# Kernel tuning notes

Measured on AMD Instinct MI355X. Metric: run time of the kernel, lower is better.

Reference implementation:

```python
import jax, jax.numpy as jnp
import numpy as np

N_HEADS = 16


def setup_inputs() -> dict:
    key = jax.random.key(0)
    k1, k2, k3 = jax.random.split(key, 3)
    d = 1024
    x = jax.random.normal(k1, (8, 1024, d), dtype=jnp.float32)
    w_qkv = jax.random.normal(k2, (d, 3 * d), dtype=jnp.float32) * (1.0 / np.sqrt(d))
    w_out = jax.random.normal(k3, (d, d), dtype=jnp.float32) * (1.0 / np.sqrt(d))
    b_out = jnp.zeros((d,), dtype=jnp.float32)
    return {"x": x, "w_qkv": w_qkv, "w_out": w_out, "b_out": b_out}


def reference(x, w_qkv, w_out, b_out):
    a, b, c = x.shape
    h = N_HEADS
    hd = c // h
    scale = 1.0 / (c ** 0.5)  # note: 1/sqrt(model_dim), not head_dim
    qkv = (x @ w_qkv).reshape(a, b, 3, h, hd)
    q, k, v = jnp.moveaxis(qkv, 2, 0)          # each (a, b, h, hd)
    q = jnp.swapaxes(q, 1, 2)                  # (a, h, b, hd)
    k = jnp.swapaxes(k, 1, 2)
    v = jnp.swapaxes(v, 1, 2)
    scores = jnp.einsum('ahqd,ahkd->ahqk', q, k) * scale  # (a, h, b, b)
    # Faithful to the source: softmax over dim=1 (the HEADS axis)
    attn = jax.nn.softmax(scores, axis=1)
    out = jnp.einsum('ahqk,ahkd->ahqd', attn, v)           # (a, h, b, hd)
    out = jnp.swapaxes(out, 1, 2).reshape(a, b, c)
    return out @ w_out + b_out
```

## Files before the change

### kernel.cpp

```cpp
#include <hip/hip_runtime.h>
#include <hip/hip_bf16.h>

typedef __attribute__((ext_vector_type(8))) short short8;
typedef __attribute__((ext_vector_type(4))) short short4e;
typedef __attribute__((ext_vector_type(4))) float f32x4;
typedef __attribute__((ext_vector_type(16))) float f32x16;
typedef __attribute__((ext_vector_type(4))) unsigned uint4v;

#define SC_LOG2E 0.04508422f
#define MFMA32(a, b, c) __builtin_amdgcn_mfma_f32_32x32x16_bf16(a, b, c, 0, 0, 0)

__device__ inline short bf16r(float f) {
    union { float f; unsigned u; } v; v.f = f;
    unsigned r = v.u + 0x7FFFu + ((v.u >> 16) & 1u);
    return (short)(r >> 16);
}
__device__ inline float bflo(unsigned u) {
    union { unsigned u; float f; } v; v.u = u << 16; return v.f;
}
__device__ inline float bfhi(unsigned u) {
    union { unsigned u; float f; } v; v.u = u & 0xffff0000u; return v.f;
}
#if __has_builtin(__builtin_amdgcn_exp2f)
__device__ inline float fexp2(float x) { return __builtin_amdgcn_exp2f(x); }
#else
__device__ inline float fexp2(float x) { return __expf(x * 0.6931471806f); }
#endif
__device__ inline unsigned cvt_pk_bf16(float lo, float hi) {
    unsigned r;
    asm("v_cvt_pk_bf16_f32 %0, %1, %2" : "=v"(r) : "v"(lo), "v"(hi));
    return r;
}
__device__ inline void perm32swap(unsigned& a, unsigned& b) {
    asm("v_permlane32_swap_b32 %0, %1" : "+v"(a), "+v"(b));
}

#define GLOAD_LDS16(gp, lp) __builtin_amdgcn_global_load_lds( \
    (const __attribute__((address_space(1))) unsigned int*)(gp), \
    (__attribute__((address_space(3))) unsigned int*)(lp), 16, 0, 0)

#define WB10 do { asm volatile("s_waitcnt vmcnt(10)\ns_barrier" ::: "memory"); __builtin_amdgcn_sched_barrier(0); } while (0)
#define WB4  do { asm volatile("s_waitcnt vmcnt(4)\ns_barrier"  ::: "memory"); __builtin_amdgcn_sched_barrier(0); } while (0)
#define WB0  do { asm volatile("s_waitcnt vmcnt(0)\ns_barrier"  ::: "memory"); __builtin_amdgcn_sched_barrier(0); } while (0)

__global__ void castk(const float* __restrict__ in, short* __restrict__ out, int n4) {
    int i = blockIdx.x * 256 + threadIdx.x;
    if (i < n4) {
        float4 v = ((const float4*)in)[i];
        short4 o;
        o.x = bf16r(v.x); o.y = bf16r(v.y); o.z = bf16r(v.z); o.w = bf16r(v.w);
        ((short4*)out)[i] = o;
    }
}

__global__ void tcast(const float* __restrict__ src, short* __restrict__ dst, int R, int C,
                      int nscale, float sfac) {
    __shared__ float tile[32][33];
    int bi = blockIdx.x, bj = blockIdx.y;
    int tx = threadIdx.x & 31, ty = threadIdx.x >> 5;
#pragma unroll
    for (int p = 0; p < 4; p++)
        tile[ty + p * 8][tx] = src[(long)(bi * 32 + ty + p * 8) * C + bj * 32 + tx];
    __syncthreads();
#pragma unroll
    for (int p = 0; p < 4; p++) {
        int n = bj * 32 + ty + p * 8;
        float v = tile[tx][ty + p * 8];
        if (n < nscale) v *= sfac;
        dst[(long)n * R + bi * 32 + tx] = bf16r(v);
    }
}

__global__ __launch_bounds__(512, 2)
void gemm256(const short* __restrict__ A, const short* __restrict__ Bt,
             short* __restrict__ qkv, short* __restrict__ Vt) {
    __shared__ short lds[65536];
    const int wg = blockIdx.x;
    const int lg = (wg & 7) * 48 + (wg >> 3);
    const int bx = lg % 12, by = lg / 12;
    const int m0 = by * 256, n0 = bx * 256;
    const int tid = threadIdx.x, w = tid >> 6, lane = tid & 63;
    const int wm = w >> 2, wn = w & 3;
    const int l15 = lane & 15, lhi = lane >> 4;
    f32x4 acc[8][4] = {};

    auto stA = [&](int t, int ks) {
#pragma unroll
        for (int j = 0; j < 2; j++) {
            int c = j * 512 + tid;
            int row = c >> 2, sl = c & 3;
            GLOAD_LDS16(A + (long)(m0 + row) * 1024 + t * 64 + ks * 32 + ((sl ^ ((row >> 1) & 3)) * 8),
                        &lds[((t & 1) * 2 + ks) * 8192 + c * 8]);
        }
    };
    auto stB = [&](int t, int ks) {
#pragma unroll
        for (int j = 0; j < 2; j++) {
            int c = j * 512 + tid;
            int row = c >> 2, sl = c & 3;
            GLOAD_LDS16(Bt + (long)(n0 + row) * 1024 + t * 64 + ks * 32 + ((sl ^ ((row >> 1) & 3)) * 8),
                        &lds[32768 + ((t & 1) * 2 + ks) * 8192 + c * 8]);
        }
    };

    short8 af[8], bf[2];
    auto ldA = [&](int buf, int ks) {
#pragma unroll
        for (int fi = 0; fi < 8; fi++) {
            int row = wm * 128 + fi * 16 + l15;
            af[fi] = *(const short8*)(&lds[(buf * 2 + ks) * 8192 + row * 32 +
                                           ((lhi ^ ((row >> 1) & 3)) * 8)]);
        }
    };
    auto ldB = [&](int buf, int ks, int fh) {
#pragma unroll
        for (int u = 0; u < 2; u++) {
            int row = wn * 64 + (fh * 2 + u) * 16 + l15;
            bf[u] = *(const short8*)(&lds[32768 + (buf * 2 + ks) * 8192 + row * 32 +
                                          ((lhi ^ ((row >> 1) & 3)) * 8)]);
        }
    };
    auto mm = [&](int fh) {
        __builtin_amdgcn_s_setprio(1);
#pragma unroll
        for (int fi = 0; fi < 8; fi++)
#pragma unroll
            for (int u = 0; u < 2; u++)
                acc[fi][fh * 2 + u] = __builtin_amdgcn_mfma_f32_16x16x32_bf16(
                    af[fi], bf[u], acc[fi][fh * 2 + u], 0, 0, 0);
        __builtin_amdgcn_s_setprio(0);
    };

    stA(0, 0); stB(0, 0); stA(0, 1); stB(0, 1); stA(1, 0); stB(1, 0);

    for (int i = 0; i < 8; i++) {
        const int t0 = 2 * i;
        stA(t0 + 1, 1); WB10;
        ldA(0, 0); ldB(0, 0, 0); mm(0);
        stB(t0 + 1, 1); WB10;
        ldB(0, 0, 1); mm(1);
        if (i < 7) stA(t0 + 2, 0);
        WB10;
        ldA(0, 1); ldB(0, 1, 0); mm(0);
        if (i < 7) stB(t0 + 2, 0);
        WB10;
        ldB(0, 1, 1); mm(1);
        if (i < 7) { stA(t0 + 2, 1); WB10; } else { WB4; }
        ldA(1, 0); ldB(1, 0, 0); mm(0);
        if (i < 7) { stB(t0 + 2, 1); WB10; } else { WB4; }
        ldB(1, 0, 1); mm(1);
        if (i < 7) { stA(t0 + 3, 0); WB10; } else { WB0; }
        ldA(1, 1); ldB(1, 1, 0); mm(0);
        if (i < 7) { stB(t0 + 3, 0); WB10; } else { WB0; }
        ldB(1, 1, 1); mm(1);
    }

    if (n0 >= 2048) {
        const int a = m0 >> 10, k0v = m0 & 1023;
#pragma unroll
        for (int fi = 0; fi < 8; fi++)
#pragma unroll
            for (int fj = 0; fj < 4; fj++) {
                int colp = n0 - 2048 + wn * 64 + fj * 16 + l15;
                int k = k0v + wm * 128 + fi * 16 + lhi * 4;
                short4e s4;
#pragma unroll
                for (int r = 0; r < 4; r++) s4[r] = bf16r(acc[fi][fj][r]);
                *(short4e*)(Vt + (long)a * 1048576 + (long)colp * 1024 + k) = s4;
            }
    } else {
#pragma unroll
        for (int fi = 0; fi < 8; fi++)
#pragma unroll
            for (int fj = 0; fj < 4; fj++)
#pragma unroll
                for (int r = 0; r < 4; r++) {
                    int row = m0 + wm * 128 + fi * 16 + lhi * 4 + r;
                    int col = n0 + wn * 64 + fj * 16 + l15;
                    qkv[(long)row * 3072 + col] = bf16r(acc[fi][fj][r]);
                }
    }
}

template<int OUT_BF16>
__global__ __launch_bounds__(256, 3)
void gemm_bt(const short* __restrict__ A, const short* __restrict__ Bt,
             void* __restrict__ Cout, const float* __restrict__ bias,
             int M, int N, int K, int nbx, int cpx, int lda) {
    __shared__ short As[3][128 * 32];
    __shared__ short Bs[3][128 * 32];
    const int wg = blockIdx.x;
    const int lg = (wg & 7) * cpx + (wg >> 3);
    const int bx = lg % nbx, by = lg / nbx;
    const int tid = threadIdx.x, w = tid >> 6, lane = tid & 63;
    const int wr = w >> 1, wc = w & 1;
    const int l15 = lane & 15, lhi = lane >> 4;
    const int m0 = by * 128, n0 = bx * 128;
    f32x4 acc[4][4] = {};
    const int NT = K / 32;

    auto stage = [&](int buf, int t) {
        int k0 = t * 32;
#pragma unroll
        for (int j = 0; j < 2; j++) {
            int chunk = w * 128 + j * 64 + lane;
            int row = chunk >> 2, cp = chunk & 3;
            int cc = cp ^ ((row >> 1) & 3);
            GLOAD_LDS16(A  + (long)(m0 + row) * lda + k0 + cc * 8, &As[buf][chunk * 8]);
            GLOAD_LDS16(Bt + (long)(n0 + row) * K   + k0 + cc * 8, &Bs[buf][chunk * 8]);
        }
    };

    stage(0, 0);
    stage(1, 1);
    asm volatile("s_waitcnt vmcnt(4)\ns_barrier" ::: "memory");
    __builtin_amdgcn_sched_barrier(0);

    int bR = 0, bW = 2;
    for (int t = 0; t < NT; t++) {
        bool issued = (t + 2 < NT);
        if (issued) stage(bW, t + 2);
        const short* Ab = As[bR];
        const short* Bb = Bs[bR];
        short8 af[4], bfr[4];
#pragma unroll
        for (int i = 0; i < 4; i++) {
            int arow = wr * 64 + i * 16 + l15;
            int brow = wc * 64 + i * 16 + l15;
            af[i]  = *(const short8*)(Ab + arow * 32 + (lhi ^ ((arow >> 1) & 3)) * 8);
            bfr[i] = *(const short8*)(Bb + brow * 32 + (lhi ^ ((brow >> 1) & 3)) * 8);
        }
        __builtin_amdgcn_s_setprio(1);
#pragma unroll
        for (int i = 0; i < 4; i++)
#pragma unroll
            for (int j = 0; j < 4; j++)
                acc[i][j] = __builtin_amdgcn_mfma_f32_16x16x32_bf16(af[i], bfr[j], acc[i][j], 0, 0, 0);
        __builtin_amdgcn_s_setprio(0);
        if (issued) asm volatile("s_waitcnt vmcnt(4)\ns_barrier" ::: "memory");
        else        asm volatile("s_waitcnt vmcnt(0)\ns_barrier" ::: "memory");
        __builtin_amdgcn_sched_barrier(0);
        bR = (bR == 2) ? 0 : bR + 1;
        bW = (bW == 2) ? 0 : bW + 1;
    }
#pragma unroll
    for (int i = 0; i < 4; i++)
#pragma unroll
        for (int j = 0; j < 4; j++)
#pragma unroll
            for (int r = 0; r < 4; r++) {
                int row = m0 + wr * 64 + i * 16 + lhi * 4 + r;
                int col = n0 + wc * 64 + j * 16 + l15;
                float v = acc[i][j][r];
                if (OUT_BF16) ((short*)Cout)[(long)row * N + col] = bf16r(v);
                else          ((float*)Cout)[(long)row * N + col] = v + bias[col];
            }
}

__global__ __launch_bounds__(256, 2)
void dsum_kernel(const short* __restrict__ qkv, unsigned* __restrict__ negL) {
    __shared__ short Qs[2][128 * 64];
    __shared__ short Ks[2][128 * 64];
    const int wg = blockIdx.x;
    const int lg = (wg & 7) * 64 + (wg >> 3);
    const int a = lg >> 6, q0 = ((lg >> 3) & 7) * 128, k0 = (lg & 7) * 128;
    const int tid = threadIdx.x, w = tid >> 6, lane = tid & 63;
    const int wr = w >> 1, wc = w & 1;
    const int l31 = lane & 31, hi = lane >> 5;
    const long qb = (long)a * 3145728;
    f32x16 dacc[2][2] = {};

    auto stage = [&](int buf, int hh) {
#pragma unroll
        for (int j = 0; j < 4; j++) {
            int c = j * 256 + tid;
            int row = c >> 3, cc = (c & 7) ^ (row & 7);
            GLOAD_LDS16(qkv + qb + (long)(q0 + row) * 3072 + hh * 64 + cc * 8,        &Qs[buf][c * 8]);
            GLOAD_LDS16(qkv + qb + (long)(k0 + row) * 3072 + 1024 + hh * 64 + cc * 8, &Ks[buf][c * 8]);
        }
    };

    stage(0, 0);
    __syncthreads();
    int buf = 0;
    for (int hh = 0; hh < 16; hh++) {
        if (hh < 15) stage(buf ^ 1, hh + 1);
        short8 ka[2][4], qf[2][4];
#pragma unroll
        for (int i = 0; i < 2; i++)
#pragma unroll
            for (int dc = 0; dc < 4; dc++) {
                int row = wr * 64 + i * 32 + l31;
                int ph = (dc * 2 + hi) ^ (row & 7);
                ka[i][dc] = *(const short8*)(&Ks[buf][row * 64 + ph * 8]);
            }
#pragma unroll
        for (int j = 0; j < 2; j++)
#pragma unroll
            for (int dc = 0; dc < 4; dc++) {
                int row = wc * 64 + j * 32 + l31;
                int ph = (dc * 2 + hi) ^ (row & 7);
                qf[j][dc] = *(const short8*)(&Qs[buf][row * 64 + ph * 8]);
            }
#pragma unroll
        for (int i = 0; i < 2; i++)
#pragma unroll
            for (int j = 0; j < 2; j++) {
                f32x16 s = {};
#pragma unroll
                for (int dc = 0; dc < 4; dc++)
                    s = MFMA32(ka[i][dc], qf[j][dc], s);
#pragma unroll
                for (int r = 0; r < 16; r++)
                    dacc[i][j][r] += fexp2(s[r]);
            }
        __syncthreads();
        buf ^= 1;
    }
#pragma unroll
    for (int i = 0; i < 2; i++)
#pragma unroll
        for (int j = 0; j < 2; j++) {
            int ktg = (k0 >> 5) + wr * 2 + i;
            int qtg = (q0 >> 5) + wc * 2 + j;
            unsigned pwv[8];
#pragma unroll
            for (int u = 0; u < 8; u++)
                pwv[u] = cvt_pk_bf16(-__log2f(dacc[i][j][2 * u]),
                                     -__log2f(dacc[i][j][2 * u + 1]));
            unsigned* dst = negL + (((long)(a * 32 + ktg) * 32 + qtg) << 9) + lane * 8;
            *(uint4v*)dst       = (uint4v){pwv[0], pwv[1], pwv[2], pwv[3]};
            *(uint4v*)(dst + 4) = (uint4v){pwv[4], pwv[5], pwv[6], pwv[7]};
        }
}

__global__ __launch_bounds__(256, 2)
void attn2_kernel(const short* __restrict__ qkv, const short* __restrict__ Vt,
                  const unsigned* __restrict__ negL, short* __restrict__ ctx) {
    __shared__ short lds[3 * 8192];
    const int wg = blockIdx.x;
    const int lg = (wg & 7) * 64 + (wg >> 3);
    const int a = lg >> 6, h = (lg >> 2) & 15, qblk = lg & 3;
    const int tid = threadIdx.x, w = tid >> 6, lane = tid & 63;
    const int l31 = lane & 31, hi = lane >> 5;
    const int qw = qblk * 256 + w * 64;
    const long qb = (long)a * 3145728;

    short8 qfrag[2][4];
#pragma unroll
    for (int qs = 0; qs < 2; qs++)
#pragma unroll
        for (int dc = 0; dc < 4; dc++)
            qfrag[qs][dc] = *(const short8*)(qkv + qb +
                (long)(qw + qs * 32 + l31) * 3072 + h * 64 + dc * 16 + hi * 8);

    const short* kcol  = qkv + qb + 1024 + h * 64;
    const short* vbase = Vt + (long)a * 1048576 + (long)(h * 64) * 1024;
    const unsigned* lbase = negL + (long)a * 524288 + (qw >> 5) * 512 + lane * 8;

    auto stage = [&](int buf, int t) {
        int k0 = t * 64;
#pragma unroll
        for (int j = 0; j < 2; j++) {
            GLOAD_LDS16(kcol + (long)(k0 + j * 32 + l31) * 3072 + w * 16 + hi * 8,
                        &lds[buf * 8192 + (j * 256 + tid) * 8]);
            int fidx = j * 4 + w, n = fidx >> 1, dt = fidx & 1;
            GLOAD_LDS16(vbase + (long)(dt * 32 + l31) * 1024 + k0 + n * 16 + hi * 8,
                        &lds[buf * 8192 + 4096 + (j * 256 + tid) * 8]);
        }
    };

    f32x16 oacc[2][2] = {};
    stage(0, 0);
    stage(1, 1);
    asm volatile("s_waitcnt vmcnt(4)\ns_barrier" ::: "memory");
    __builtin_amdgcn_sched_barrier(0);

    int bR = 0, bW = 2;
    for (int t = 0; t < 16; t++) {
        uint4v dm[2][2][2];
#pragma unroll
        for (int qs = 0; qs < 2; qs++)
#pragma unroll
            for (int kt = 0; kt < 2; kt++) {
                const unsigned* dp = lbase + (long)(t * 2 + kt) * 16384 + qs * 512;
                dm[qs][kt][0] = *(const uint4v*)dp;
                dm[qs][kt][1] = *(const uint4v*)(dp + 4);
            }
        if (t + 2 < 16) stage(bW, t + 2);

        const short* Kb = &lds[bR * 8192];
        const short* Vb = &lds[bR * 8192 + 4096];
#pragma unroll
        for (int kt = 0; kt < 2; kt++) {
            short8 ka[4];
#pragma unroll
            for (int dc = 0; dc < 4; dc++)
                ka[dc] = *(const short8*)(Kb + ((kt * 4 + dc) * 64 + lane) * 8);

            short8 pf[2][2];
#pragma unroll
            for (int qs = 0; qs < 2; qs++) {
                f32x16 s = {};
                __builtin_amdgcn_s_setprio(1);
#pragma unroll
                for (int dc = 0; dc < 4; dc++)
                    s = MFMA32(ka[dc], qfrag[qs][dc], s);
                __builtin_amdgcn_s_setprio(0);
                unsigned pw[8];
#pragma unroll
                for (int u = 0; u < 8; u++) {
                    unsigned d = dm[qs][kt][u >> 2][u & 3];
                    float e0 = fexp2(s[2 * u]     + bflo(d));
                    float e1 = fexp2(s[2 * u + 1] + bfhi(d));
                    pw[u] = cvt_pk_bf16(e0, e1);
                }
                perm32swap(pw[0], pw[2]); perm32swap(pw[1], pw[3]);
                perm32swap(pw[4], pw[6]); perm32swap(pw[5], pw[7]);
                union { uint4v u; short8 s8; } c0, c1;
                c0.u = (uint4v){pw[0], pw[1], pw[2], pw[3]};
                c1.u = (uint4v){pw[4], pw[5], pw[6], pw[7]};
                pf[qs][0] = c0.s8;
                pf[qs][1] = c1.s8;
            }
            __builtin_amdgcn_s_setprio(1);
#pragma unroll
            for (int dt = 0; dt < 2; dt++)
#pragma unroll
                for (int nn = 0; nn < 2; nn++) {
                    short8 vf = *(const short8*)(Vb + (((kt * 2 + nn) * 2 + dt) * 64 + lane) * 8);
#pragma unroll
                    for (int qs = 0; qs < 2; qs++)
                        oacc[qs][dt] = MFMA32(pf[qs][nn], vf, oacc[qs][dt]);
                }
            __builtin_amdgcn_s_setprio(0);
        }
        asm volatile("s_waitcnt vmcnt(4)\ns_barrier" ::: "memory");
        __builtin_amdgcn_sched_barrier(0);
        bR = (bR == 2) ? 0 : bR + 1;
        bW = (bW == 2) ? 0 : bW + 1;
    }
#pragma unroll
    for (int qs = 0; qs < 2; qs++)
#pragma unroll
        for (int dt = 0; dt < 2; dt++)
#pragma unroll
            for (int r = 0; r < 16; r++) {
                int q = qw + qs * 32 + (r & 3) + 8 * (r >> 2) + 4 * hi;
                int col = h * 64 + dt * 32 + l31;
                ctx[((long)a * 1024 + q) * 3072 + col] = bf16r(oacc[qs][dt][r]);
            }
}

extern "C" void kernel_launch(void* const* d_in, const int* in_sizes, int n_in,
                              void* d_out, int out_size, void* d_ws, size_t ws_size,
                              hipStream_t stream) {
    const float* x     = (const float*)d_in[0];
    const float* w_qkv = (const float*)d_in[1];
    const float* w_out = (const float*)d_in[2];
    const float* b_out = (const float*)d_in[3];
    float* out = (float*)d_out;

    char* ws = (char*)d_ws;
    short* wqkvT   = (short*)(ws);
    unsigned* negL = (unsigned*)(ws);
    short* xb    = (short*)(ws + 16777216);
    short* woT   = (short*)(ws + 33554432);
    short* qkv   = (short*)(ws + 35651584);
    short* Vt    = (short*)(ws + 85983232);
    short* ctx   = qkv + 2048;
    if (ws_size < 109051904u) return;

    castk<<<8192, 256, 0, stream>>>(x, xb, 2097152);
    tcast<<<dim3(32, 96), 256, 0, stream>>>(w_qkv, wqkvT, 1024, 3072, 1024, SC_LOG2E);
    tcast<<<dim3(32, 32), 256, 0, stream>>>(w_out, woT, 1024, 1024, 0, 1.0f);
    gemm256<<<384, 512, 0, stream>>>(xb, wqkvT, qkv, Vt);
    dsum_kernel<<<512, 256, 0, stream>>>(qkv, negL);
    attn2_kernel<<<512, 256, 0, stream>>>(qkv, Vt, negL, ctx);
    gemm_bt<0><<<512, 256, 0, stream>>>(ctx, woT, (void*)out, b_out, 8192, 1024, 1024, 8, 64, 3072);
}
```

Baseline: 192.5 us.

## Widen QKV GEMM tile to 256x384 so 256 workgroups fill the GPU in one wave

The QKV projection GEMM now uses 256x384 output tiles, which gives 256 workgroups that map one per CU on the 256-CU part instead of 384 tiles running in 1.5 waves. LDS grows to hold the larger B tile, occupancy drops to one workgroup per CU, and the software pipeline is rewritten with a per-k-tile schedule, new vmcnt waits and plain barriers. The epilogue now picks the Vt or qkv store per 16-column fragment, because a tile can straddle the V boundary. The risks are the lost latency hiding from the second resident workgroup and possible errors in the hand-tuned wait counts.

```diff
diff --git a/kernel.cpp b/kernel.cpp
--- a/kernel.cpp
+++ b/kernel.cpp
@@ -39,9 +39,12 @@
     (const __attribute__((address_space(1))) unsigned int*)(gp), \
     (__attribute__((address_space(3))) unsigned int*)(lp), 16, 0, 0)
 
+#define WB12 do { asm volatile("s_waitcnt vmcnt(12)\ns_barrier" ::: "memory"); __builtin_amdgcn_sched_barrier(0); } while (0)
 #define WB10 do { asm volatile("s_waitcnt vmcnt(10)\ns_barrier" ::: "memory"); __builtin_amdgcn_sched_barrier(0); } while (0)
+#define WB5  do { asm volatile("s_waitcnt vmcnt(5)\ns_barrier"  ::: "memory"); __builtin_amdgcn_sched_barrier(0); } while (0)
 #define WB4  do { asm volatile("s_waitcnt vmcnt(4)\ns_barrier"  ::: "memory"); __builtin_amdgcn_sched_barrier(0); } while (0)
 #define WB0  do { asm volatile("s_waitcnt vmcnt(0)\ns_barrier"  ::: "memory"); __builtin_amdgcn_sched_barrier(0); } while (0)
+#define BARO do { asm volatile("s_barrier" ::: "memory"); __builtin_amdgcn_sched_barrier(0); } while (0)
 
 __global__ void castk(const float* __restrict__ in, short* __restrict__ out, int n4) {
     int i = blockIdx.x * 256 + threadIdx.x;
@@ -71,18 +74,19 @@
     }
 }
 
-__global__ __launch_bounds__(512, 2)
+__global__ __launch_bounds__(512, 1)
 void gemm256(const short* __restrict__ A, const short* __restrict__ Bt,
              short* __restrict__ qkv, short* __restrict__ Vt) {
-    __shared__ short lds[65536];
+    __shared__ short lds[81920];
     const int wg = blockIdx.x;
-    const int lg = (wg & 7) * 48 + (wg >> 3);
-    const int bx = lg % 12, by = lg / 12;
-    const int m0 = by * 256, n0 = bx * 256;
+    const int cx = wg & 7, idx = wg >> 3;
+    const int by = (cx & 3) * 8 + (idx & 7);
+    const int bx = (cx >> 2) * 4 + (idx >> 3);
+    const int m0 = by * 256, n0 = bx * 384;
     const int tid = threadIdx.x, w = tid >> 6, lane = tid & 63;
     const int wm = w >> 2, wn = w & 3;
     const int l15 = lane & 15, lhi = lane >> 4;
-    f32x4 acc[8][4] = {};
+    f32x4 acc[8][6] = {};
 
     auto stA = [&](int t, int ks) {
 #pragma unroll
@@ -95,11 +99,11 @@
     };
     auto stB = [&](int t, int ks) {
 #pragma unroll
-        for (int j = 0; j < 2; j++) {
+        for (int j = 0; j < 3; j++) {
             int c = j * 512 + tid;
             int row = c >> 2, sl = c & 3;
             GLOAD_LDS16(Bt + (long)(n0 + row) * 1024 + t * 64 + ks * 32 + ((sl ^ ((row >> 1) & 3)) * 8),
-                        &lds[32768 + ((t & 1) * 2 + ks) * 8192 + c * 8]);
+                        &lds[32768 + ((t & 1) * 2 + ks) * 12288 + c * 8]);
         }
     };
 
@@ -115,8 +119,8 @@
     auto ldB = [&](int buf, int ks, int fh) {
 #pragma unroll
         for (int u = 0; u < 2; u++) {
-            int row = wn * 64 + (fh * 2 + u) * 16 + l15;
-            bf[u] = *(const short8*)(&lds[32768 + (buf * 2 + ks) * 8192 + row * 32 +
+            int row = wn * 96 + (fh * 2 + u) * 16 + l15;
+            bf[u] = *(const short8*)(&lds[32768 + (buf * 2 + ks) * 12288 + row * 32 +
                                           ((lhi ^ ((row >> 1) & 3)) * 8)]);
         }
     };
@@ -131,55 +135,55 @@
         __builtin_amdgcn_s_setprio(0);
     };
 
-    stA(0, 0); stB(0, 0); stA(0, 1); stB(0, 1); stA(1, 0); stB(1, 0);
-
-    for (int i = 0; i < 8; i++) {
-        const int t0 = 2 * i;
-        stA(t0 + 1, 1); WB10;
-        ldA(0, 0); ldB(0, 0, 0); mm(0);
-        stB(t0 + 1, 1); WB10;
-        ldB(0, 0, 1); mm(1);
-        if (i < 7) stA(t0 + 2, 0);
-        WB10;
-        ldA(0, 1); ldB(0, 1, 0); mm(0);
-        if (i < 7) stB(t0 + 2, 0);
-        WB10;
-        ldB(0, 1, 1); mm(1);
-        if (i < 7) { stA(t0 + 2, 1); WB10; } else { WB4; }
-        ldA(1, 0); ldB(1, 0, 0); mm(0);
-        if (i < 7) { stB(t0 + 2, 1); WB10; } else { WB4; }
-        ldB(1, 0, 1); mm(1);
-        if (i < 7) { stA(t0 + 3, 0); WB10; } else { WB0; }
-        ldA(1, 1); ldB(1, 1, 0); mm(0);
-        if (i < 7) { stB(t0 + 3, 0); WB10; } else { WB0; }
-        ldB(1, 1, 1); mm(1);
-    }
-
-    if (n0 >= 2048) {
-        const int a = m0 >> 10, k0v = m0 & 1023;
-#pragma unroll
-        for (int fi = 0; fi < 8; fi++)
-#pragma unroll
-            for (int fj = 0; fj < 4; fj++) {
-                int colp = n0 - 2048 + wn * 64 + fj * 16 + l15;
+    stA(0, 0); stB(0, 0); stA(0, 1); stB(0, 1); stA(1, 0); stB(1, 0); stA(1, 1);
+
+    for (int t = 0; t < 14; t++) {
+        const int b = t & 1;
+        WB12;             ldA(b, 0); ldB(b, 0, 0); mm(0);
+        stB(t + 1, 1); BARO; ldB(b, 0, 1); mm(1);
+        stA(t + 2, 0); BARO; ldB(b, 0, 2); mm(2);
+        WB12;             ldA(b, 1); ldB(b, 1, 0); mm(0);
+        stB(t + 2, 0); BARO; ldB(b, 1, 1); mm(1);
+        stA(t + 2, 1); BARO; ldB(b, 1, 2); mm(2);
+    }
+    {
+        WB12;             ldA(0, 0); ldB(0, 0, 0); mm(0);
+        stB(15, 1); BARO; ldB(0, 0, 1); mm(1);
+        BARO;             ldB(0, 0, 2); mm(2);
+        WB10;             ldA(0, 1); ldB(0, 1, 0); mm(0);
+        BARO;             ldB(0, 1, 1); mm(1);
+        BARO;             ldB(0, 1, 2); mm(2);
+    }
+    {
+        WB5;              ldA(1, 0); ldB(1, 0, 0); mm(0);
+        BARO;             ldB(1, 0, 1); mm(1);
+        BARO;             ldB(1, 0, 2); mm(2);
+        WB0;              ldA(1, 1); ldB(1, 1, 0); mm(0);
+        BARO;             ldB(1, 1, 1); mm(1);
+        BARO;             ldB(1, 1, 2); mm(2);
+    }
+
+    const int a = m0 >> 10, k0v = m0 & 1023;
+#pragma unroll
+    for (int fi = 0; fi < 8; fi++)
+#pragma unroll
+        for (int fj = 0; fj < 6; fj++) {
+            int colb = n0 + wn * 96 + fj * 16;
+            if (colb >= 2048) {
+                int colp = colb - 2048 + l15;
                 int k = k0v + wm * 128 + fi * 16 + lhi * 4;
                 short4e s4;
 #pragma unroll
                 for (int r = 0; r < 4; r++) s4[r] = bf16r(acc[fi][fj][r]);
                 *(short4e*)(Vt + (long)a * 1048576 + (long)colp * 1024 + k) = s4;
-            }
-    } else {
-#pragma unroll
-        for (int fi = 0; fi < 8; fi++)
-#pragma unroll
-            for (int fj = 0; fj < 4; fj++)
+            } else {
 #pragma unroll
                 for (int r = 0; r < 4; r++) {
                     int row = m0 + wm * 128 + fi * 16 + lhi * 4 + r;
-                    int col = n0 + wn * 64 + fj * 16 + l15;
-                    qkv[(long)row * 3072 + col] = bf16r(acc[fi][fj][r]);
+                    qkv[(long)row * 3072 + colb + l15] = bf16r(acc[fi][fj][r]);
                 }
-    }
+            }
+        }
 }
 
 template<int OUT_BF16>
@@ -474,7 +478,7 @@
     castk<<<8192, 256, 0, stream>>>(x, xb, 2097152);
     tcast<<<dim3(32, 96), 256, 0, stream>>>(w_qkv, wqkvT, 1024, 3072, 1024, SC_LOG2E);
     tcast<<<dim3(32, 32), 256, 0, stream>>>(w_out, woT, 1024, 1024, 0, 1.0f);
-    gemm256<<<384, 512, 0, stream>>>(xb, wqkvT, qkv, Vt);
+    gemm256<<<256, 512, 0, stream>>>(xb, wqkvT, qkv, Vt);
     dsum_kernel<<<512, 256, 0, stream>>>(qkv, negL);
     attn2_kernel<<<512, 256, 0, stream>>>(qkv, Vt, negL, ctx);
     gemm_bt<0><<<512, 256, 0, stream>>>(ctx, woT, (void*)out, b_out, 8192, 1024, 1024, 8, 64, 3072);
```

New measurement: 202.8 us. 5.3% more time.
